# Optimization experiments

Measured on AMD Instinct MI355X. Metric: run time of the kernel, lower is better.

The kernel has to match this reference:

```python
import jax, jax.numpy as jnp
import numpy as np

B, T, D = 8, 2048, 512


def setup_inputs() -> dict:
    key = jax.random.key(0)
    ks = jax.random.split(key, 12)
    s = 1.0 / np.sqrt(D)
    return {
        "x": jax.random.normal(ks[0], (B, T, D), dtype=jnp.float32),
        "Wq": jax.random.normal(ks[1], (D, D), dtype=jnp.float32) * s,
        "bq": jax.random.normal(ks[2], (D,), dtype=jnp.float32) * 0.01,
        "Wk": jax.random.normal(ks[3], (D, D), dtype=jnp.float32) * s,
        "bk": jax.random.normal(ks[4], (D,), dtype=jnp.float32) * 0.01,
        "Wv": jax.random.normal(ks[5], (D, D), dtype=jnp.float32) * s,
        "bv": jax.random.normal(ks[6], (D,), dtype=jnp.float32) * 0.01,
        "Wbeta": jax.random.normal(ks[7], (1, D), dtype=jnp.float32) * s,
        "bbeta": jax.random.normal(ks[8], (1,), dtype=jnp.float32) * 0.01,
        "Wo": jax.random.normal(ks[9], (D, D), dtype=jnp.float32) * s,
        "bo": jax.random.normal(ks[10], (D,), dtype=jnp.float32) * 0.01,
    }


def _l2_normalize(v, eps=1e-12):
    # torch F.normalize(p=2, dim=-1): v / max(||v||, eps)
    n = jnp.sqrt(jnp.sum(v * v, axis=-1, keepdims=True))
    return v / jnp.maximum(n, eps)


def _deltanet(x, Wq, bq, Wk, bk, Wv, bv, Wbeta, bbeta, Wo, bo):
    Q = x @ Wq.T + bq                      # [B,T,D]
    K = _l2_normalize(x @ Wk.T + bk)       # [B,T,D], unit-norm keys
    V = x @ Wv.T + bv                      # [B,T,D]
    Beta = jax.nn.sigmoid(K @ Wbeta.T + bbeta)  # [B,T,1]

    # time-major for scan: [T,B,D] / [T,B,1]
    Qt = jnp.swapaxes(Q, 0, 1)
    Kt = jnp.swapaxes(K, 0, 1)
    Vt = jnp.swapaxes(V, 0, 1)
    Bt = jnp.swapaxes(Beta, 0, 1)

    S0 = jnp.zeros((x.shape[0], x.shape[-1], x.shape[-1]), dtype=x.dtype)

    def step(S, inp):
        q, k, v, beta = inp                 # [B,D],[B,D],[B,D],[B,1]
        Sk = jnp.einsum("bij,bj->bi", S, k)           # S k_t
        b = beta[:, :, None]                            # [B,1,1]
        # S_t = S - beta (S k) k^T + beta v k^T
        S = S - b * (Sk[:, :, None] * k[:, None, :]) + b * (v[:, :, None] * k[:, None, :])
        o = jnp.einsum("bij,bj->bi", S, q)              # o_t = S_t q_t
        return S, o

    _, Ot = jax.lax.scan(step, S0, (Qt, Kt, Vt, Bt))    # [T,B,D]
    O = jnp.swapaxes(Ot, 0, 1)                          # [B,T,D]
    return O @ Wo.T + bo


def reference(x, Wq, bq, Wk, bk, Wv, bv, Wbeta, bbeta, Wo, bo):
    return _deltanet(x, Wq, bq, Wk, bk, Wv, bv, Wbeta, bbeta, Wo, bo)
```

## Files before the change

### kernel.cpp

```cpp
#include <hip/hip_runtime.h>

#define D 512
#define T 2048
#define BATCH 8
#define M_ROWS (BATCH*T)
#define CHK 64
#define NCHB 32
#define NCHUNK 256

typedef __attribute__((ext_vector_type(8))) short short8;
typedef __attribute__((ext_vector_type(4))) float floatx4;

__device__ __forceinline__ unsigned short f2bf(float f) {
  unsigned int u = __float_as_uint(f);
  u += 0x7FFFu + ((u >> 16) & 1u);
  return (unsigned short)(u >> 16);
}
__device__ __forceinline__ float bf2f(unsigned int h) {
  return __uint_as_float(h << 16);
}
__device__ __forceinline__ float wave_allreduce(float v) {
  #pragma unroll
  for (int m = 32; m; m >>= 1) v += __shfl_xor(v, m, 64);
  return v;
}
__device__ __forceinline__ void unpack8(uint4 r, float f[8]) {
  f[0] = bf2f(r.x & 0xffffu); f[1] = bf2f(r.x >> 16);
  f[2] = bf2f(r.y & 0xffffu); f[3] = bf2f(r.y >> 16);
  f[4] = bf2f(r.z & 0xffffu); f[5] = bf2f(r.z >> 16);
  f[6] = bf2f(r.w & 0xffffu); f[7] = bf2f(r.w >> 16);
}

__global__ __launch_bounds__(256) void cast_kernel(const float* __restrict__ src,
                                                   unsigned short* __restrict__ dst, int n) {
  int idx = (blockIdx.x * 256 + threadIdx.x) * 8;
  if (idx >= n) return;
  const float4* sp = (const float4*)(src + idx);
  float4 a = sp[0], b = sp[1];
  uint4 o;
  o.x = f2bf(a.x) | ((unsigned)f2bf(a.y) << 16);
  o.y = f2bf(a.z) | ((unsigned)f2bf(a.w) << 16);
  o.z = f2bf(b.x) | ((unsigned)f2bf(b.y) << 16);
  o.w = f2bf(b.z) | ((unsigned)f2bf(b.w) << 16);
  *(uint4*)(dst + idx) = o;
}

#define BM 128
#define BN 128
#define BK 32

template<bool OUT_BF16>
__global__ __launch_bounds__(256) void gemm_nt(
    const unsigned short* __restrict__ A, const unsigned short* __restrict__ Bw,
    const float* __restrict__ bias, void* __restrict__ Cout, int M, int N, int K)
{
  __shared__ __align__(16) unsigned short As[BM * BK];
  __shared__ __align__(16) unsigned short Bs[BN * BK];
  int tid  = threadIdx.x;
  int lane = tid & 63;
  int wave = tid >> 6;
  int waveM = (wave >> 1) * 64;
  int waveN = (wave & 1) * 64;
  int lrow = lane & 15;
  int quad = lane >> 4;

  floatx4 acc[4][4];
  #pragma unroll
  for (int a_ = 0; a_ < 4; ++a_)
    #pragma unroll
    for (int b_ = 0; b_ < 4; ++b_) acc[a_][b_] = (floatx4){0.f, 0.f, 0.f, 0.f};

  const unsigned short* Ap = A  + (size_t)(blockIdx.y * BM) * K;
  const unsigned short* Bp = Bw + (size_t)(blockIdx.x * BN) * K;
  int r0 = tid >> 2;
  int c0 = (tid & 3) * 8;

  for (int k0 = 0; k0 < K; k0 += BK) {
    __syncthreads();
    *(uint4*)&As[r0 * BK + c0]        = *(const uint4*)&Ap[(size_t)r0 * K + k0 + c0];
    *(uint4*)&As[(r0 + 64) * BK + c0] = *(const uint4*)&Ap[(size_t)(r0 + 64) * K + k0 + c0];
    *(uint4*)&Bs[r0 * BK + c0]        = *(const uint4*)&Bp[(size_t)r0 * K + k0 + c0];
    *(uint4*)&Bs[(r0 + 64) * BK + c0] = *(const uint4*)&Bp[(size_t)(r0 + 64) * K + k0 + c0];
    __syncthreads();
    short8 af[4], bf[4];
    #pragma unroll
    for (int mt = 0; mt < 4; ++mt)
      af[mt] = *(const short8*)&As[(waveM + mt * 16 + lrow) * BK + quad * 8];
    #pragma unroll
    for (int nt = 0; nt < 4; ++nt)
      bf[nt] = *(const short8*)&Bs[(waveN + nt * 16 + lrow) * BK + quad * 8];
    #pragma unroll
    for (int mt = 0; mt < 4; ++mt)
      #pragma unroll
      for (int nt = 0; nt < 4; ++nt)
        acc[mt][nt] = __builtin_amdgcn_mfma_f32_16x16x32_bf16(af[mt], bf[nt], acc[mt][nt], 0, 0, 0);
  }

  int cm = blockIdx.y * BM + waveM;
  int cn = blockIdx.x * BN + waveN;
  #pragma unroll
  for (int nt = 0; nt < 4; ++nt) {
    int col = cn + nt * 16 + lrow;
    float bv = bias[col];
    #pragma unroll
    for (int mt = 0; mt < 4; ++mt) {
      #pragma unroll
      for (int r = 0; r < 4; ++r) {
        int row = cm + mt * 16 + quad * 4 + r;
        float v = acc[mt][nt][r] + bv;
        if (OUT_BF16) ((unsigned short*)Cout)[(size_t)row * N + col] = f2bf(v);
        else          ((float*)Cout)[(size_t)row * N + col] = v;
      }
    }
  }
}

__global__ __launch_bounds__(256) void norm_beta_kernel(
    unsigned short* __restrict__ Kb, const float* __restrict__ Wbeta,
    const float* __restrict__ bbeta, float* __restrict__ Beta)
{
  int w = blockIdx.x * 4 + (threadIdx.x >> 6);
  int lane = threadIdx.x & 63;
  unsigned short* kp = Kb + (size_t)w * D + lane * 8;
  uint4 raw = *(uint4*)kp;
  float kv[8]; unpack8(raw, kv);
  float ss = 0.f;
  #pragma unroll
  for (int m = 0; m < 8; ++m) ss += kv[m] * kv[m];
  ss = wave_allreduce(ss);
  float inv = 1.0f / fmaxf(sqrtf(ss), 1e-12f);
  const float* wb = Wbeta + lane * 8;
  float dotp = 0.f;
  #pragma unroll
  for (int m = 0; m < 8; ++m) { kv[m] *= inv; dotp += kv[m] * wb[m]; }
  uint4 o;
  o.x = f2bf(kv[0]) | ((unsigned)f2bf(kv[1]) << 16);
  o.y = f2bf(kv[2]) | ((unsigned)f2bf(kv[3]) << 16);
  o.z = f2bf(kv[4]) | ((unsigned)f2bf(kv[5]) << 16);
  o.w = f2bf(kv[6]) | ((unsigned)f2bf(kv[7]) << 16);
  *(uint4*)kp = o;
  dotp = wave_allreduce(dotp);
  if (lane == 0) Beta[w] = 1.0f / (1.0f + expf(-(dotp + bbeta[0])));
}

__global__ __launch_bounds__(256) void transpose_k(
    const unsigned short* __restrict__ Kb, unsigned short* __restrict__ KT)
{
  __shared__ __align__(16) unsigned short Kc[64 * 520];
  int cb = blockIdx.x, tid = threadIdx.x;
  const unsigned short* src = Kb + (size_t)cb * 64 * 512;
  #pragma unroll
  for (int it = 0; it < 16; ++it) {
    int e = it * 2048 + tid * 8;
    int row = e >> 9, col = e & 511;
    *(uint4*)&Kc[row * 520 + col] = *(const uint4*)&src[row * 512 + col];
  }
  __syncthreads();
  unsigned short* dst = KT + (size_t)cb * 32768;
  #pragma unroll
  for (int it = 0; it < 16; ++it) {
    int e = it * 2048 + tid * 8;
    int dk = e >> 6, t0 = e & 63;
    uint4 o;
    unsigned short tv[8];
    #pragma unroll
    for (int u = 0; u < 8; ++u) tv[u] = Kc[(t0 + u) * 520 + dk];
    o.x = tv[0] | ((unsigned)tv[1] << 16);
    o.y = tv[2] | ((unsigned)tv[3] << 16);
    o.z = tv[4] | ((unsigned)tv[5] << 16);
    o.w = tv[6] | ((unsigned)tv[7] << 16);
    *(uint4*)&dst[e] = o;
  }
}

__global__ __launch_bounds__(256) void gram_kernel(
    const unsigned short* __restrict__ Qb, const unsigned short* __restrict__ Kb,
    const float* __restrict__ Beta, float* __restrict__ Abuf,
    unsigned short* __restrict__ Msb)
{
  int cb = blockIdx.x, tid = threadIdx.x, lane = tid & 63, w = tid >> 6;
  int lr = lane & 15, quad = lane >> 4;
  const unsigned short* kc = Kb + (size_t)cb * 64 * 512;
  const unsigned short* qc = Qb + (size_t)cb * 64 * 512;
  floatx4 accK[4], accQ[4];
  #pragma unroll
  for (int nt = 0; nt < 4; ++nt) { accK[nt] = (floatx4){0,0,0,0}; accQ[nt] = (floatx4){0,0,0,0}; }
  #pragma unroll
  for (int ks = 0; ks < 16; ++ks) {
    short8 ak = *(const short8*)&kc[(w * 16 + lr) * 512 + ks * 32 + quad * 8];
    short8 aq = *(const short8*)&qc[(w * 16 + lr) * 512 + ks * 32 + quad * 8];
    short8 bk[4];
    #pragma unroll
    for (int nt = 0; nt < 4; ++nt)
      bk[nt] = *(const short8*)&kc[(nt * 16 + lr) * 512 + ks * 32 + quad * 8];
    #pragma unroll
    for (int nt = 0; nt < 4; ++nt) {
      accK[nt] = __builtin_amdgcn_mfma_f32_16x16x32_bf16(ak, bk[nt], accK[nt], 0, 0, 0);
      accQ[nt] = __builtin_amdgcn_mfma_f32_16x16x32_bf16(aq, bk[nt], accQ[nt], 0, 0, 0);
    }
  }
  #pragma unroll
  for (int nt = 0; nt < 4; ++nt)
    #pragma unroll
    for (int r = 0; r < 4; ++r) {
      int t = w * 16 + quad * 4 + r;
      int j = nt * 16 + lr;
      float bt = Beta[cb * 64 + t];
      Abuf[(size_t)cb * 4096 + t * 64 + j] = (j < t) ? bt * accK[nt][r] : 0.f;
      Msb[(size_t)cb * 4096 + t * 64 + j]  = f2bf((j <= t) ? accQ[nt][r] : 0.f);
    }
}

__global__ __launch_bounds__(256) void tinv_kernel(
    const float* __restrict__ Abuf, const float* __restrict__ Beta,
    unsigned short* __restrict__ Tib)
{
  __shared__ float XL[4 * 4096];
  int tid = threadIdx.x, w = tid >> 6, lane = tid & 63;
  int cb = blockIdx.x * 4 + w;
  float* X = XL + w * 4096;
  #pragma unroll
  for (int j = 0; j < 64; ++j) X[j * 64 + lane] = 0.f;
  float bl = Beta[cb * 64 + lane];
  const float* Ab = Abuf + (size_t)cb * 4096;
  unsigned short* To = Tib + (size_t)cb * 4096;
  for (int t = 0; t < 64; ++t) {
    float y = (lane == t) ? 1.f : 0.f;
    const float* Ar = Ab + t * 64;
    for (int jb = 0; jb < 64; jb += 8) {
      float av[8], xv[8];
      #pragma unroll
      for (int u = 0; u < 8; ++u) { av[u] = Ar[jb + u]; xv[u] = X[(jb + u) * 64 + lane]; }
      #pragma unroll
      for (int u = 0; u < 8; ++u) y = fmaf(-av[u], xv[u], y);
    }
    X[t * 64 + lane] = y;
    To[t * 64 + lane] = f2bf(y * bl);
  }
}

__global__ __launch_bounds__(256) void wu_kernel(
    const unsigned short* __restrict__ Tib, const unsigned short* __restrict__ KT,
    const unsigned short* __restrict__ Vb, unsigned short* __restrict__ Wneg,
    unsigned short* __restrict__ Ubar)
{
  __shared__ __align__(16) unsigned short Vc[64 * 520];
  int cb = blockIdx.x, tid = threadIdx.x, lane = tid & 63, w = tid >> 6;
  int lr = lane & 15, quad = lane >> 4;
  const unsigned short* vsrc = Vb + (size_t)cb * 64 * 512;
  #pragma unroll
  for (int it = 0; it < 16; ++it) {
    int e = it * 2048 + tid * 8, row = e >> 9, col = e & 511;
    *(uint4*)&Vc[row * 520 + col] = *(const uint4*)&vsrc[row * 512 + col];
  }
  __syncthreads();
  short8 af[2];
  #pragma unroll
  for (int ks = 0; ks < 2; ++ks)
    af[ks] = *(const short8*)&Tib[(size_t)cb * 4096 + (w * 16 + lr) * 64 + ks * 32 + quad * 8];
  const unsigned short* ktc = KT + (size_t)cb * 32768;
  for (int nt = 0; nt < 32; ++nt) {
    floatx4 aw = (floatx4){0,0,0,0}, au = (floatx4){0,0,0,0};
    #pragma unroll
    for (int ks = 0; ks < 2; ++ks) {
      short8 bk = *(const short8*)&ktc[(nt * 16 + lr) * 64 + ks * 32 + quad * 8];
      short8 bv;
      #pragma unroll
      for (int u = 0; u < 8; ++u)
        bv[u] = (short)Vc[(ks * 32 + quad * 8 + u) * 520 + nt * 16 + lr];
      aw = __builtin_amdgcn_mfma_f32_16x16x32_bf16(af[ks], bk, aw, 0, 0, 0);
      au = __builtin_amdgcn_mfma_f32_16x16x32_bf16(af[ks], bv, au, 0, 0, 0);
    }
    #pragma unroll
    for (int r = 0; r < 4; ++r) {
      int t = w * 16 + quad * 4 + r, dd = nt * 16 + lr;
      Wneg[((size_t)cb * 64 + t) * 512 + dd] = f2bf(-aw[r]);
      Ubar[((size_t)cb * 64 + t) * 512 + dd] = f2bf(au[r]);
    }
  }
}

__global__ __launch_bounds__(256) void seq_kernel(
    const unsigned short* __restrict__ Wneg, const unsigned short* __restrict__ Qb,
    const unsigned short* __restrict__ Ubar, const unsigned short* __restrict__ Msb,
    const unsigned short* __restrict__ KT, unsigned short* __restrict__ Ob)
{
  __shared__ __align__(16) unsigned short Sb[16 * 520];
  __shared__ __align__(16) unsigned short Ut[16 * 72];
  int blk = blockIdx.x;
  int b = blk >> 5, vs = blk & 31;
  int vg0 = vs * 16;
  int tid = threadIdx.x, lane = tid & 63, w = tid >> 6;
  int lr = lane & 15, quad = lane >> 4;
  floatx4 sacc[8];
  #pragma unroll
  for (int nt = 0; nt < 8; ++nt) sacc[nt] = (floatx4){0,0,0,0};

  for (int ch = 0; ch < NCHB; ++ch) {
    int cb = b * NCHB + ch;
    size_t tokb = (size_t)cb * 64;
    #pragma unroll
    for (int nt = 0; nt < 8; ++nt)
      #pragma unroll
      for (int r = 0; r < 4; ++r)
        Sb[(quad * 4 + r) * 520 + w * 128 + nt * 16 + lr] = f2bf(sacc[nt][r]);
    __syncthreads();
    floatx4 du;
    #pragma unroll
    for (int r = 0; r < 4; ++r)
      du[r] = bf2f(Ubar[(tokb + w * 16 + quad * 4 + r) * 512 + vg0 + lr]);
    #pragma unroll
    for (int ks = 0; ks < 16; ++ks) {
      short8 a = *(const short8*)&Wneg[(tokb + w * 16 + lr) * 512 + ks * 32 + quad * 8];
      short8 bfr = *(const short8*)&Sb[lr * 520 + ks * 32 + quad * 8];
      du = __builtin_amdgcn_mfma_f32_16x16x32_bf16(a, bfr, du, 0, 0, 0);
    }
    #pragma unroll
    for (int r = 0; r < 4; ++r)
      Ut[lr * 72 + w * 16 + quad * 4 + r] = f2bf(du[r]);
    __syncthreads();
    floatx4 doo = (floatx4){0,0,0,0};
    #pragma unroll
    for (int ks = 0; ks < 16; ++ks) {
      short8 a = *(const short8*)&Qb[(tokb + w * 16 + lr) * 512 + ks * 32 + quad * 8];
      short8 bfr = *(const short8*)&Sb[lr * 520 + ks * 32 + quad * 8];
      doo = __builtin_amdgcn_mfma_f32_16x16x32_bf16(a, bfr, doo, 0, 0, 0);
    }
    short8 a2[2];
    #pragma unroll
    for (int ks = 0; ks < 2; ++ks)
      a2[ks] = *(const short8*)&Ut[lr * 72 + ks * 32 + quad * 8];
    #pragma unroll
    for (int ks = 0; ks < 2; ++ks) {
      short8 a = *(const short8*)&Msb[(size_t)cb * 4096 + (w * 16 + lr) * 64 + ks * 32 + quad * 8];
      doo = __builtin_amdgcn_mfma_f32_16x16x32_bf16(a, a2[ks], doo, 0, 0, 0);
    }
    #pragma unroll
    for (int r = 0; r < 4; ++r)
      Ob[(tokb + w * 16 + quad * 4 + r) * 512 + vg0 + lr] = f2bf(doo[r]);
    #pragma unroll
    for (int nt = 0; nt < 8; ++nt) {
      #pragma unroll
      for (int ks = 0; ks < 2; ++ks) {
        int dk = w * 128 + nt * 16 + lr;
        short8 bfr = *(const short8*)&KT[(size_t)cb * 32768 + dk * 64 + ks * 32 + quad * 8];
        sacc[nt] = __builtin_amdgcn_mfma_f32_16x16x32_bf16(a2[ks], bfr, sacc[nt], 0, 0, 0);
      }
    }
    __syncthreads();
  }
}

extern "C" void kernel_launch(void* const* d_in, const int* in_sizes, int n_in,
                              void* d_out, int out_size, void* d_ws, size_t ws_size,
                              hipStream_t stream) {
  const float* x     = (const float*)d_in[0];
  const float* Wq    = (const float*)d_in[1];
  const float* bq    = (const float*)d_in[2];
  const float* Wk    = (const float*)d_in[3];
  const float* bk    = (const float*)d_in[4];
  const float* Wv    = (const float*)d_in[5];
  const float* bv    = (const float*)d_in[6];
  const float* Wbeta = (const float*)d_in[7];
  const float* bbeta = (const float*)d_in[8];
  const float* Wo    = (const float*)d_in[9];
  const float* bo    = (const float*)d_in[10];

  const size_t NE = (size_t)M_ROWS * D;
  const size_t DD = (size_t)D * D;
  unsigned short* Qb  = (unsigned short*)d_ws;
  unsigned short* Kb  = Qb + NE;
  unsigned short* Vb  = Kb + NE;
  unsigned short* Xb  = Vb + NE;
  unsigned short* Wqb = Xb + NE;
  unsigned short* Wkb = Wqb + DD;
  unsigned short* Wvb = Wkb + DD;
  unsigned short* Wob = Wvb + DD;
  float* Beta = (float*)(Wob + DD);
  unsigned short* KT  = (unsigned short*)(Beta + M_ROWS);
  float* Abuf = (float*)(KT + NE);
  unsigned short* Msb = (unsigned short*)(Abuf + (size_t)NCHUNK * 4096);
  unsigned short* Tib = Msb + (size_t)NCHUNK * 4096;

  cast_kernel<<<(int)(NE / 2048), 256, 0, stream>>>(x, Xb, (int)NE);
  cast_kernel<<<(int)(DD / 2048), 256, 0, stream>>>(Wq, Wqb, (int)DD);
  cast_kernel<<<(int)(DD / 2048), 256, 0, stream>>>(Wk, Wkb, (int)DD);
  cast_kernel<<<(int)(DD / 2048), 256, 0, stream>>>(Wv, Wvb, (int)DD);
  cast_kernel<<<(int)(DD / 2048), 256, 0, stream>>>(Wo, Wob, (int)DD);

  dim3 gg(D / BN, M_ROWS / BM);
  gemm_nt<true><<<gg, 256, 0, stream>>>(Xb, Wqb, bq, Qb, M_ROWS, D, D);
  gemm_nt<true><<<gg, 256, 0, stream>>>(Xb, Wkb, bk, Kb, M_ROWS, D, D);
  gemm_nt<true><<<gg, 256, 0, stream>>>(Xb, Wvb, bv, Vb, M_ROWS, D, D);

  norm_beta_kernel<<<M_ROWS / 4, 256, 0, stream>>>(Kb, Wbeta, bbeta, Beta);

  transpose_k<<<NCHUNK, 256, 0, stream>>>(Kb, KT);
  gram_kernel<<<NCHUNK, 256, 0, stream>>>(Qb, Kb, Beta, Abuf, Msb);
  tinv_kernel<<<NCHUNK / 4, 256, 0, stream>>>(Abuf, Beta, Tib);
  wu_kernel<<<NCHUNK, 256, 0, stream>>>(Tib, KT, Vb, Xb, Kb);

  seq_kernel<<<NCHUNK, 256, 0, stream>>>(Xb, Qb, Kb, Msb, KT, Vb);

  gemm_nt<false><<<gg, 256, 0, stream>>>(Vb, Wob, bo, (float*)d_out, M_ROWS, D, D);
}
```

Before: 484.3 us.

## Prefetch next-chunk operands in seq kernel and restructure WY/T-inverse kernels

The sequential chunk kernel now loads the next chunk's Wneg, Q, K^T, M and Ubar fragments into registers while the current chunk computes, splits the accumulators in two to shorten MFMA dependency chains, and drops one barrier. V is transposed alongside K so wu_kernel reads contiguous B fragments and stages its outputs in swizzled LDS for coalesced stores. tinv_kernel moves to one wave per chunk, uses a row-major X with float4 loads, and stops the inner loop at the triangular bound. The cost is much higher register pressure in seq_kernel, made explicit with launch_bounds(256,1), plus an extra VT buffer.

```diff
diff --git a/kernel.cpp b/kernel.cpp
--- a/kernel.cpp
+++ b/kernel.cpp
@@ -143,12 +143,14 @@
   if (lane == 0) Beta[w] = 1.0f / (1.0f + expf(-(dotp + bbeta[0])));
 }
 
-__global__ __launch_bounds__(256) void transpose_k(
-    const unsigned short* __restrict__ Kb, unsigned short* __restrict__ KT)
+__global__ __launch_bounds__(256) void transpose_kv(
+    const unsigned short* __restrict__ Kb, const unsigned short* __restrict__ Vb,
+    unsigned short* __restrict__ KT, unsigned short* __restrict__ VT)
 {
   __shared__ __align__(16) unsigned short Kc[64 * 520];
-  int cb = blockIdx.x, tid = threadIdx.x;
-  const unsigned short* src = Kb + (size_t)cb * 64 * 512;
+  int cb = blockIdx.x & 255, tid = threadIdx.x;
+  const unsigned short* src = (blockIdx.x < 256 ? Kb : Vb) + (size_t)cb * 64 * 512;
+  unsigned short* dst = (blockIdx.x < 256 ? KT : VT) + (size_t)cb * 32768;
   #pragma unroll
   for (int it = 0; it < 16; ++it) {
     int e = it * 2048 + tid * 8;
@@ -156,7 +158,6 @@
     *(uint4*)&Kc[row * 520 + col] = *(const uint4*)&src[row * 512 + col];
   }
   __syncthreads();
-  unsigned short* dst = KT + (size_t)cb * 32768;
   #pragma unroll
   for (int it = 0; it < 16; ++it) {
     int e = it * 2048 + tid * 8;
@@ -211,76 +212,83 @@
     }
 }
 
-__global__ __launch_bounds__(256) void tinv_kernel(
+__global__ __launch_bounds__(64) void tinv_kernel(
     const float* __restrict__ Abuf, const float* __restrict__ Beta,
     unsigned short* __restrict__ Tib)
 {
-  __shared__ float XL[4 * 4096];
-  int tid = threadIdx.x, w = tid >> 6, lane = tid & 63;
-  int cb = blockIdx.x * 4 + w;
-  float* X = XL + w * 4096;
-  #pragma unroll
-  for (int j = 0; j < 64; ++j) X[j * 64 + lane] = 0.f;
+  __shared__ float XT[64 * 68];
+  int lane = threadIdx.x;
+  int cb = blockIdx.x;
   float bl = Beta[cb * 64 + lane];
   const float* Ab = Abuf + (size_t)cb * 4096;
   unsigned short* To = Tib + (size_t)cb * 4096;
+  float* Xr = XT + lane * 68;
+  #pragma unroll
+  for (int j = 0; j < 68; j += 4) *(float4*)&Xr[j] = (float4){0.f,0.f,0.f,0.f};
   for (int t = 0; t < 64; ++t) {
-    float y = (lane == t) ? 1.f : 0.f;
     const float* Ar = Ab + t * 64;
-    for (int jb = 0; jb < 64; jb += 8) {
-      float av[8], xv[8];
-      #pragma unroll
-      for (int u = 0; u < 8; ++u) { av[u] = Ar[jb + u]; xv[u] = X[(jb + u) * 64 + lane]; }
-      #pragma unroll
-      for (int u = 0; u < 8; ++u) y = fmaf(-av[u], xv[u], y);
-    }
-    X[t * 64 + lane] = y;
+    float p0 = 0.f, p1 = 0.f, p2 = 0.f, p3 = 0.f;
+    for (int jb = 0; jb < t; jb += 4) {
+      float4 xv = *(const float4*)&Xr[jb];
+      float4 av = *(const float4*)&Ar[jb];
+      p0 = fmaf(av.x, xv.x, p0); p1 = fmaf(av.y, xv.y, p1);
+      p2 = fmaf(av.z, xv.z, p2); p3 = fmaf(av.w, xv.w, p3);
+    }
+    float y = ((lane == t) ? 1.f : 0.f) - (p0 + p1) - (p2 + p3);
+    Xr[t] = y;
     To[t * 64 + lane] = f2bf(y * bl);
   }
 }
 
 __global__ __launch_bounds__(256) void wu_kernel(
     const unsigned short* __restrict__ Tib, const unsigned short* __restrict__ KT,
-    const unsigned short* __restrict__ Vb, unsigned short* __restrict__ Wneg,
+    const unsigned short* __restrict__ VT, unsigned short* __restrict__ Wneg,
     unsigned short* __restrict__ Ubar)
 {
-  __shared__ __align__(16) unsigned short Vc[64 * 520];
+  __shared__ __align__(16) unsigned short WL[64 * 512];
+  __shared__ __align__(16) unsigned short UL[64 * 512];
   int cb = blockIdx.x, tid = threadIdx.x, lane = tid & 63, w = tid >> 6;
   int lr = lane & 15, quad = lane >> 4;
-  const unsigned short* vsrc = Vb + (size_t)cb * 64 * 512;
+  short8 af0 = *(const short8*)&Tib[(size_t)cb * 4096 + (w * 16 + lr) * 64 + quad * 8];
+  short8 af1 = *(const short8*)&Tib[(size_t)cb * 4096 + (w * 16 + lr) * 64 + 32 + quad * 8];
+  const unsigned short* ktc = KT + (size_t)cb * 32768 + lr * 64 + quad * 8;
+  const unsigned short* vtc = VT + (size_t)cb * 32768 + lr * 64 + quad * 8;
+  int tbase = w * 16 + quad * 4;
+  #pragma unroll 4
+  for (int nt = 0; nt < 32; ++nt) {
+    short8 bk0 = *(const short8*)(ktc + nt * 1024);
+    short8 bk1 = *(const short8*)(ktc + nt * 1024 + 32);
+    short8 bv0 = *(const short8*)(vtc + nt * 1024);
+    short8 bv1 = *(const short8*)(vtc + nt * 1024 + 32);
+    floatx4 z = (floatx4){0.f,0.f,0.f,0.f};
+    floatx4 aw = __builtin_amdgcn_mfma_f32_16x16x32_bf16(af0, bk0, z, 0, 0, 0);
+    aw = __builtin_amdgcn_mfma_f32_16x16x32_bf16(af1, bk1, aw, 0, 0, 0);
+    floatx4 au = __builtin_amdgcn_mfma_f32_16x16x32_bf16(af0, bv0, z, 0, 0, 0);
+    au = __builtin_amdgcn_mfma_f32_16x16x32_bf16(af1, bv1, au, 0, 0, 0);
+    int bi = nt * 2 + (lr >> 3);
+    int lo = lr & 7;
+    #pragma unroll
+    for (int r = 0; r < 4; ++r) {
+      int tt = tbase + r;
+      int bis = bi ^ (tt & 7);
+      WL[tt * 512 + bis * 8 + lo] = f2bf(-aw[r]);
+      UL[tt * 512 + bis * 8 + lo] = f2bf(au[r]);
+    }
+  }
+  __syncthreads();
+  unsigned short* wd = Wneg + (size_t)cb * 32768;
+  unsigned short* ud = Ubar + (size_t)cb * 32768;
   #pragma unroll
   for (int it = 0; it < 16; ++it) {
-    int e = it * 2048 + tid * 8, row = e >> 9, col = e & 511;
-    *(uint4*)&Vc[row * 520 + col] = *(const uint4*)&vsrc[row * 512 + col];
-  }
-  __syncthreads();
-  short8 af[2];
-  #pragma unroll
-  for (int ks = 0; ks < 2; ++ks)
-    af[ks] = *(const short8*)&Tib[(size_t)cb * 4096 + (w * 16 + lr) * 64 + ks * 32 + quad * 8];
-  const unsigned short* ktc = KT + (size_t)cb * 32768;
-  for (int nt = 0; nt < 32; ++nt) {
-    floatx4 aw = (floatx4){0,0,0,0}, au = (floatx4){0,0,0,0};
-    #pragma unroll
-    for (int ks = 0; ks < 2; ++ks) {
-      short8 bk = *(const short8*)&ktc[(nt * 16 + lr) * 64 + ks * 32 + quad * 8];
-      short8 bv;
-      #pragma unroll
-      for (int u = 0; u < 8; ++u)
-        bv[u] = (short)Vc[(ks * 32 + quad * 8 + u) * 520 + nt * 16 + lr];
-      aw = __builtin_amdgcn_mfma_f32_16x16x32_bf16(af[ks], bk, aw, 0, 0, 0);
-      au = __builtin_amdgcn_mfma_f32_16x16x32_bf16(af[ks], bv, au, 0, 0, 0);
-    }
-    #pragma unroll
-    for (int r = 0; r < 4; ++r) {
-      int t = w * 16 + quad * 4 + r, dd = nt * 16 + lr;
-      Wneg[((size_t)cb * 64 + t) * 512 + dd] = f2bf(-aw[r]);
-      Ubar[((size_t)cb * 64 + t) * 512 + dd] = f2bf(au[r]);
-    }
-  }
-}
-
-__global__ __launch_bounds__(256) void seq_kernel(
+    int e = it * 2048 + tid * 8;
+    int row = e >> 9, col = e & 511;
+    int bis = (col >> 3) ^ (row & 7);
+    *(uint4*)&wd[e] = *(const uint4*)&WL[row * 512 + bis * 8];
+    *(uint4*)&ud[e] = *(const uint4*)&UL[row * 512 + bis * 8];
+  }
+}
+
+__global__ __launch_bounds__(256, 1) void seq_kernel(
     const unsigned short* __restrict__ Wneg, const unsigned short* __restrict__ Qb,
     const unsigned short* __restrict__ Ubar, const unsigned short* __restrict__ Msb,
     const unsigned short* __restrict__ KT, unsigned short* __restrict__ Ob)
@@ -292,62 +300,90 @@
   int vg0 = vs * 16;
   int tid = threadIdx.x, lane = tid & 63, w = tid >> 6;
   int lr = lane & 15, quad = lane >> 4;
+
   floatx4 sacc[8];
   #pragma unroll
-  for (int nt = 0; nt < 8; ++nt) sacc[nt] = (floatx4){0,0,0,0};
+  for (int nt = 0; nt < 8; ++nt) sacc[nt] = (floatx4){0.f,0.f,0.f,0.f};
+
+  short8 wn[16], qf[16], kt[16], ms[2];
+  unsigned short ub[4];
+
+  auto LD_WQ = [&](int cb) {
+    const unsigned short* wr = Wneg + ((size_t)cb * 64 + w * 16 + lr) * 512 + quad * 8;
+    const unsigned short* qr = Qb   + ((size_t)cb * 64 + w * 16 + lr) * 512 + quad * 8;
+    #pragma unroll
+    for (int ks = 0; ks < 16; ++ks) {
+      wn[ks] = *(const short8*)(wr + ks * 32);
+      qf[ks] = *(const short8*)(qr + ks * 32);
+    }
+  };
+  auto LD_KM = [&](int cb) {
+    const unsigned short* kr = KT + (size_t)cb * 32768 + (w * 128 + lr) * 64 + quad * 8;
+    #pragma unroll
+    for (int nt = 0; nt < 8; ++nt) {
+      kt[nt * 2 + 0] = *(const short8*)(kr + nt * 1024);
+      kt[nt * 2 + 1] = *(const short8*)(kr + nt * 1024 + 32);
+    }
+    const unsigned short* mr = Msb + (size_t)cb * 4096 + (w * 16 + lr) * 64 + quad * 8;
+    ms[0] = *(const short8*)(mr);
+    ms[1] = *(const short8*)(mr + 32);
+  };
+  auto LD_UB = [&](int cb) {
+    const unsigned short* ur = Ubar + ((size_t)cb * 64 + w * 16 + quad * 4) * 512 + vg0 + lr;
+    #pragma unroll
+    for (int r = 0; r < 4; ++r) ub[r] = ur[r * 512];
+  };
+
+  int cb0 = b * NCHB;
+  LD_WQ(cb0); LD_KM(cb0); LD_UB(cb0);
 
   for (int ch = 0; ch < NCHB; ++ch) {
-    int cb = b * NCHB + ch;
-    size_t tokb = (size_t)cb * 64;
+    int cb = cb0 + ch;
+    int cbn = cb0 + (ch + 1 < NCHB ? ch + 1 : ch);
     #pragma unroll
     for (int nt = 0; nt < 8; ++nt)
       #pragma unroll
       for (int r = 0; r < 4; ++r)
         Sb[(quad * 4 + r) * 520 + w * 128 + nt * 16 + lr] = f2bf(sacc[nt][r]);
     __syncthreads();
-    floatx4 du;
+    floatx4 du0, du1, do0, do1;
+    #pragma unroll
+    for (int r = 0; r < 4; ++r) du0[r] = bf2f(ub[r]);
+    du1 = (floatx4){0.f,0.f,0.f,0.f};
+    do0 = (floatx4){0.f,0.f,0.f,0.f};
+    do1 = (floatx4){0.f,0.f,0.f,0.f};
+    #pragma unroll
+    for (int ks = 0; ks < 16; ++ks) {
+      short8 sb = *(const short8*)&Sb[lr * 520 + ks * 32 + quad * 8];
+      if (ks & 1) {
+        du1 = __builtin_amdgcn_mfma_f32_16x16x32_bf16(wn[ks], sb, du1, 0, 0, 0);
+        do1 = __builtin_amdgcn_mfma_f32_16x16x32_bf16(qf[ks], sb, do1, 0, 0, 0);
+      } else {
+        du0 = __builtin_amdgcn_mfma_f32_16x16x32_bf16(wn[ks], sb, du0, 0, 0, 0);
+        do0 = __builtin_amdgcn_mfma_f32_16x16x32_bf16(qf[ks], sb, do0, 0, 0, 0);
+      }
+    }
     #pragma unroll
     for (int r = 0; r < 4; ++r)
-      du[r] = bf2f(Ubar[(tokb + w * 16 + quad * 4 + r) * 512 + vg0 + lr]);
-    #pragma unroll
-    for (int ks = 0; ks < 16; ++ks) {
-      short8 a = *(const short8*)&Wneg[(tokb + w * 16 + lr) * 512 + ks * 32 + quad * 8];
-      short8 bfr = *(const short8*)&Sb[lr * 520 + ks * 32 + quad * 8];
-      du = __builtin_amdgcn_mfma_f32_16x16x32_bf16(a, bfr, du, 0, 0, 0);
-    }
-    #pragma unroll
-    for (int r = 0; r < 4; ++r)
-      Ut[lr * 72 + w * 16 + quad * 4 + r] = f2bf(du[r]);
+      Ut[lr * 72 + w * 16 + quad * 4 + r] = f2bf(du0[r] + du1[r]);
+    LD_WQ(cbn);
+    LD_UB(cbn);
     __syncthreads();
-    floatx4 doo = (floatx4){0,0,0,0};
-    #pragma unroll
-    for (int ks = 0; ks < 16; ++ks) {
-      short8 a = *(const short8*)&Qb[(tokb + w * 16 + lr) * 512 + ks * 32 + quad * 8];
-      short8 bfr = *(const short8*)&Sb[lr * 520 + ks * 32 + quad * 8];
-      doo = __builtin_amdgcn_mfma_f32_16x16x32_bf16(a, bfr, doo, 0, 0, 0);
-    }
-    short8 a2[2];
-    #pragma unroll
-    for (int ks = 0; ks < 2; ++ks)
-      a2[ks] = *(const short8*)&Ut[lr * 72 + ks * 32 + quad * 8];
-    #pragma unroll
-    for (int ks = 0; ks < 2; ++ks) {
-      short8 a = *(const short8*)&Msb[(size_t)cb * 4096 + (w * 16 + lr) * 64 + ks * 32 + quad * 8];
-      doo = __builtin_amdgcn_mfma_f32_16x16x32_bf16(a, a2[ks], doo, 0, 0, 0);
-    }
-    #pragma unroll
-    for (int r = 0; r < 4; ++r)
-      Ob[(tokb + w * 16 + quad * 4 + r) * 512 + vg0 + lr] = f2bf(doo[r]);
+    short8 a2_0 = *(const short8*)&Ut[lr * 72 + quad * 8];
+    short8 a2_1 = *(const short8*)&Ut[lr * 72 + 32 + quad * 8];
+    do0 = __builtin_amdgcn_mfma_f32_16x16x32_bf16(ms[0], a2_0, do0, 0, 0, 0);
+    do1 = __builtin_amdgcn_mfma_f32_16x16x32_bf16(ms[1], a2_1, do1, 0, 0, 0);
     #pragma unroll
     for (int nt = 0; nt < 8; ++nt) {
+      sacc[nt] = __builtin_amdgcn_mfma_f32_16x16x32_bf16(a2_0, kt[nt * 2 + 0], sacc[nt], 0, 0, 0);
+      sacc[nt] = __builtin_amdgcn_mfma_f32_16x16x32_bf16(a2_1, kt[nt * 2 + 1], sacc[nt], 0, 0, 0);
+    }
+    {
+      unsigned short* ob = Ob + ((size_t)cb * 64 + w * 16 + quad * 4) * 512 + vg0 + lr;
       #pragma unroll
-      for (int ks = 0; ks < 2; ++ks) {
-        int dk = w * 128 + nt * 16 + lr;
-        short8 bfr = *(const short8*)&KT[(size_t)cb * 32768 + dk * 64 + ks * 32 + quad * 8];
-        sacc[nt] = __builtin_amdgcn_mfma_f32_16x16x32_bf16(a2[ks], bfr, sacc[nt], 0, 0, 0);
-      }
-    }
-    __syncthreads();
+      for (int r = 0; r < 4; ++r) ob[r * 512] = f2bf(do0[r] + do1[r]);
+    }
+    LD_KM(cbn);
   }
 }
 
@@ -381,6 +417,7 @@
   float* Abuf = (float*)(KT + NE);
   unsigned short* Msb = (unsigned short*)(Abuf + (size_t)NCHUNK * 4096);
   unsigned short* Tib = Msb + (size_t)NCHUNK * 4096;
+  unsigned short* VT  = Tib + (size_t)NCHUNK * 4096;
 
   cast_kernel<<<(int)(NE / 2048), 256, 0, stream>>>(x, Xb, (int)NE);
   cast_kernel<<<(int)(DD / 2048), 256, 0, stream>>>(Wq, Wqb, (int)DD);
@@ -395,10 +432,10 @@
 
   norm_beta_kernel<<<M_ROWS / 4, 256, 0, stream>>>(Kb, Wbeta, bbeta, Beta);
 
-  transpose_k<<<NCHUNK, 256, 0, stream>>>(Kb, KT);
+  transpose_kv<<<2 * NCHUNK, 256, 0, stream>>>(Kb, Vb, KT, VT);
   gram_kernel<<<NCHUNK, 256, 0, stream>>>(Qb, Kb, Beta, Abuf, Msb);
-  tinv_kernel<<<NCHUNK / 4, 256, 0, stream>>>(Abuf, Beta, Tib);
-  wu_kernel<<<NCHUNK, 256, 0, stream>>>(Tib, KT, Vb, Xb, Kb);
+  tinv_kernel<<<NCHUNK, 64, 0, stream>>>(Abuf, Beta, Tib);
+  wu_kernel<<<NCHUNK, 256, 0, stream>>>(Tib, KT, VT, Xb, Kb);
 
   seq_kernel<<<NCHUNK, 256, 0, stream>>>(Xb, Qb, Kb, Msb, KT, Vb);
 
```

Result: no change. 478.7 us (-1.2%).
